# Kernel optimization log

Measured on AMD Instinct MI355X. Metric: run time of the kernel, lower is better.

The kernel has to match this reference:

```python
import jax, jax.numpy as jnp
import numpy as np

N = 50000          # nodes
E = 800000         # edges (avg degree 16)
IN, HID, OUT = 128, 32, 64
H1, H2, H3 = 4, 4, 6
NEG_SLOPE = 0.2


def setup_inputs() -> dict:
    key = jax.random.key(0)
    ks = jax.random.split(key, 18)

    def p(k, shape, fan_in):
        return (jax.random.normal(k, shape, jnp.float32) / np.sqrt(fan_in)).astype(jnp.float32)

    return {
        "x": jax.random.normal(ks[0], (N, IN), jnp.float32),
        "src": jax.random.randint(ks[1], (E,), 0, N, jnp.int32),
        "dst": jax.random.randint(ks[2], (E,), 0, N, jnp.int32),
        # layer 1: IN -> (H1, HID)
        "W1": p(ks[3], (IN, H1 * HID), IN),
        "al1": p(ks[4], (H1, HID), HID),
        "ar1": p(ks[5], (H1, HID), HID),
        "b1": jnp.zeros((H1 * HID,), jnp.float32),
        # layer 2: H1*HID -> (H2, HID), residual (identity since H1*HID == H2*HID... == in)
        "W2": p(ks[6], (H1 * HID, H2 * HID), H1 * HID),
        "al2": p(ks[7], (H2, HID), HID),
        "ar2": p(ks[8], (H2, HID), HID),
        "b2": jnp.zeros((H2 * HID,), jnp.float32),
        # layer 3: H2*HID -> (H3, OUT), residual via linear projection
        "W3": p(ks[9], (H2 * HID, H3 * OUT), H2 * HID),
        "al3": p(ks[10], (H3, OUT), OUT),
        "ar3": p(ks[11], (H3, OUT), OUT),
        "b3": jnp.zeros((H3 * OUT,), jnp.float32),
        "Wres3": p(ks[12], (H2 * HID, H3 * OUT), H2 * HID),
    }


def _gat_layer(h, W, al, ar, b, src, dst, H, D, resval=None):
    # DGL GATConv: proj, per-edge attention logits, leaky-relu, edge softmax
    # over destination neighborhoods, weighted gather-scatter aggregation.
    feat = (h @ W).reshape(N, H, D)                     # [N,H,D]
    el = jnp.sum(feat * al, axis=-1)                    # [N,H]
    er = jnp.sum(feat * ar, axis=-1)                    # [N,H]
    e = jax.nn.leaky_relu(el[src] + er[dst], NEG_SLOPE) # [E,H]
    # numerically-stable segment softmax over dst
    m = jax.ops.segment_max(e, dst, num_segments=N)     # [N,H]
    ex = jnp.exp(e - m[dst])
    s = jax.ops.segment_sum(ex, dst, num_segments=N)    # [N,H]
    a = ex / s[dst]                                     # [E,H]
    msg = feat[src] * a[..., None]                      # [E,H,D]
    rst = jax.ops.segment_sum(msg, dst, num_segments=N) # [N,H,D]
    if resval is not None:
        rst = rst + resval
    return rst + b.reshape(1, H, D)


def reference(x, src, dst, W1, al1, ar1, b1, W2, al2, ar2, b2,
              W3, al3, ar3, b3, Wres3):
    h = jax.nn.elu(_gat_layer(x, W1, al1, ar1, b1, src, dst, H1, HID))
    h = h.reshape(N, H1 * HID)
    h2 = jax.nn.elu(_gat_layer(h, W2, al2, ar2, b2, src, dst, H2, HID,
                               resval=h.reshape(N, H2, HID)))
    h2 = h2.reshape(N, H2 * HID)
    h3 = _gat_layer(h2, W3, al3, ar3, b3, src, dst, H3, OUT,
                    resval=(h2 @ Wres3).reshape(N, H3, OUT))
    return h3.mean(axis=1)                              # [N,OUT]
```

## Files before the change

kernel.cpp:

```cpp
#include <hip/hip_runtime.h>
#include <hip/hip_bf16.h>


#define NODES 50000
#define EDGES 800000
#define NEG 0.2f

typedef __attribute__((ext_vector_type(8))) short bh8;
typedef __attribute__((ext_vector_type(4))) float f4;

__device__ __forceinline__ float leaky(float e) { return e > 0.f ? e : NEG * e; }
__device__ __forceinline__ float blo(unsigned u) { return __uint_as_float(u << 16); }
__device__ __forceinline__ float bhi(unsigned u) { return __uint_as_float(u & 0xffff0000u); }
__device__ __forceinline__ unsigned f2bf(float f) {
    unsigned u = __float_as_uint(f);
    return (u + 0x7fffu + ((u >> 16) & 1u)) >> 16;
}
__device__ __forceinline__ void pk2(float a, float b, unsigned& hi, unsigned& lo) {
    unsigned ha = f2bf(a), hb = f2bf(b);
    float ra = a - __uint_as_float(ha << 16);
    float rb = b - __uint_as_float(hb << 16);
    hi = ha | (hb << 16);
    lo = f2bf(ra) | (f2bf(rb) << 16);
}

#define SW(row, bc) (((row) << 8) + ((bc) ^ (((row) & 7) << 4)))

__global__ void k_cast(const float* __restrict__ in, unsigned short* __restrict__ outb, int n4) {
    int gid = blockIdx.x * blockDim.x + threadIdx.x;
    if (gid >= n4) return;
    float4 v = *reinterpret_cast<const float4*>(in + (size_t)gid * 4);
    unsigned u0 = f2bf(v.x) | (f2bf(v.y) << 16);
    unsigned u1 = f2bf(v.z) | (f2bf(v.w) << 16);
    *reinterpret_cast<uint2*>(outb + (size_t)gid * 4) = make_uint2(u0, u1);
}

__global__ void k_prepw(const float* __restrict__ W, unsigned short* __restrict__ WT, int F) {
    int gid = blockIdx.x * blockDim.x + threadIdx.x;
    if (gid >= 128 * F) return;
    int k = gid / F, f = gid - k * F;
    WT[(size_t)f * 128 + k] = (unsigned short)f2bf(W[gid]);
}

__global__ void k_prep_bt2(const float* __restrict__ W3, const float* __restrict__ Wres3,
                           unsigned short* __restrict__ BT2) {
    int gid = blockIdx.x * blockDim.x + threadIdx.x;
    if (gid >= 64 * 896) return;
    int d = gid / 896, k = gid - d * 896;
    float v;
    if (k < 768) {
        v = W3[(size_t)(k & 127) * 384 + (k >> 7) * 64 + d];
    } else {
        int kr = k - 768;
        v = 0.f;
#pragma unroll
        for (int h = 0; h < 6; ++h) v += Wres3[(size_t)kr * 384 + h * 64 + d];
    }
    BT2[(size_t)d * 896 + k] = (unsigned short)f2bf(v);
}

__global__ void k_prep_alr3(const float* __restrict__ W3, const float* __restrict__ al3,
                            const float* __restrict__ ar3, float* __restrict__ al3c,
                            float* __restrict__ ar3c) {
    int gid = blockIdx.x * blockDim.x + threadIdx.x;
    if (gid >= 1536) return;
    int g = (gid < 768) ? gid : gid - 768;
    int h = g >> 7, k = g & 127;
    const float* a = (gid < 768) ? al3 : ar3;
    float s = 0.f;
#pragma unroll
    for (int d = 0; d < 64; ++d) s += W3[(size_t)k * 384 + h * 64 + d] * a[h * 64 + d];
    if (gid < 768) al3c[g] = s; else ar3c[g] = s;
}

__global__ void k_prep_mb(const float* __restrict__ b3, float* __restrict__ mb) {
    int d = threadIdx.x;
    if (d >= 64) return;
    float s = 0.f;
#pragma unroll
    for (int h = 0; h < 6; ++h) s += b3[h * 64 + d];
    mb[d] = s * (1.f / 6.f);
}

__global__ void k_hist2(const int* __restrict__ dst, int* __restrict__ cnt,
                        int* __restrict__ rank, int e) {
    int gid = blockIdx.x * blockDim.x + threadIdx.x;
    if (gid < e) rank[gid] = atomicAdd(&cnt[dst[gid]], 1);
}

__global__ void k_bsum(const int* __restrict__ deg, int* __restrict__ bsum, int n) {
    __shared__ int sm[256];
    int t = threadIdx.x;
    int i = blockIdx.x * 256 + t;
    sm[t] = (i < n) ? deg[i] : 0;
    __syncthreads();
#pragma unroll
    for (int off = 128; off > 0; off >>= 1) {
        if (t < off) sm[t] += sm[t + off];
        __syncthreads();
    }
    if (t == 0) bsum[blockIdx.x] = sm[0];
}

__global__ void k_bscan(const int* __restrict__ bsum, int* __restrict__ bpre, int nb) {
    __shared__ int sm[256];
    int t = threadIdx.x;
    int v = (t < nb) ? bsum[t] : 0;
    sm[t] = v;
    __syncthreads();
    for (int off = 1; off < 256; off <<= 1) {
        int u = (t >= off) ? sm[t - off] : 0;
        __syncthreads();
        sm[t] += u;
        __syncthreads();
    }
    if (t < nb) bpre[t] = sm[t] - v;
}

__global__ void k_offs(const int* __restrict__ deg, const int* __restrict__ bpre,
                       int* __restrict__ offs, int n, int e) {
    __shared__ int sm[256];
    int t = threadIdx.x;
    int i = blockIdx.x * 256 + t;
    int v = (i < n) ? deg[i] : 0;
    sm[t] = v;
    __syncthreads();
    for (int off = 1; off < 256; off <<= 1) {
        int u = (t >= off) ? sm[t - off] : 0;
        __syncthreads();
        sm[t] += u;
        __syncthreads();
    }
    if (i < n) offs[i] = bpre[blockIdx.x] + sm[t] - v;
    if (i == 0) offs[n] = e;
}

__global__ void k_fill2(const int* __restrict__ src, const int* __restrict__ dst,
                        const int* __restrict__ offs, const int* __restrict__ rank,
                        int2* __restrict__ csr2, int e) {
    int gid = blockIdx.x * blockDim.x + threadIdx.x;
    if (gid < e) {
        int d = dst[gid];
        int pos = offs[d] + rank[gid];
        csr2[pos] = make_int2(src[gid], d);
    }
}

__global__ void k_ew4(const int2* __restrict__ csr2, const float* __restrict__ el,
                      const float* __restrict__ er, unsigned short* __restrict__ aw, int e) {
    int gid = blockIdx.x * blockDim.x + threadIdx.x;
    if (gid >= e) return;
    int2 sd = csr2[gid];
    float4 l4 = *reinterpret_cast<const float4*>(el + (size_t)sd.x * 4);
    float4 r4 = *reinterpret_cast<const float4*>(er + (size_t)sd.y * 4);
    float w0 = __expf(leaky(l4.x + r4.x));
    float w1 = __expf(leaky(l4.y + r4.y));
    float w2 = __expf(leaky(l4.z + r4.z));
    float w3 = __expf(leaky(l4.w + r4.w));
    unsigned u0 = f2bf(w0) | (f2bf(w1) << 16);
    unsigned u1 = f2bf(w2) | (f2bf(w3) << 16);
    *reinterpret_cast<uint2*>(aw + (size_t)gid * 4) = make_uint2(u0, u1);
}

__global__ void k_ew6(const int2* __restrict__ csr2, const float* __restrict__ el,
                      const float* __restrict__ er, unsigned short* __restrict__ aw, int e) {
    int gid = blockIdx.x * blockDim.x + threadIdx.x;
    if (gid >= e) return;
    int2 sd = csr2[gid];
    const float2* lp = reinterpret_cast<const float2*>(el + (size_t)sd.x * 6);
    const float2* rp = reinterpret_cast<const float2*>(er + (size_t)sd.y * 6);
    float2 l0 = lp[0], l1 = lp[1], l2 = lp[2];
    float2 r0 = rp[0], r1 = rp[1], r2 = rp[2];
    unsigned w01 = f2bf(__expf(leaky(l0.x + r0.x))) | (f2bf(__expf(leaky(l0.y + r0.y))) << 16);
    unsigned w23 = f2bf(__expf(leaky(l1.x + r1.x))) | (f2bf(__expf(leaky(l1.y + r1.y))) << 16);
    unsigned w45 = f2bf(__expf(leaky(l2.x + r2.x))) | (f2bf(__expf(leaky(l2.y + r2.y))) << 16);
    unsigned char* wb = reinterpret_cast<unsigned char*>(aw) + (size_t)gid * 12;
    *reinterpret_cast<unsigned*>(wb + 0) = w01;
    *reinterpret_cast<unsigned*>(wb + 4) = w23;
    *reinterpret_cast<unsigned*>(wb + 8) = w45;
}

__global__ void k_denom4(const unsigned short* __restrict__ aw,
                         const int* __restrict__ offs, float* __restrict__ inv4, int n) {
    int gid = blockIdx.x * blockDim.x + threadIdx.x;
    if (gid >= n) return;
    int o0 = offs[gid], o1 = offs[gid + 1];
    float s0 = 0.f, s1 = 0.f, s2 = 0.f, s3 = 0.f;
    for (int p = o0; p < o1; ++p) {
        uint2 wu = *reinterpret_cast<const uint2*>(aw + (size_t)p * 4);
        s0 += blo(wu.x); s1 += bhi(wu.x);
        s2 += blo(wu.y); s3 += bhi(wu.y);
    }
    float4 r = (o1 > o0) ? make_float4(1.f / s0, 1.f / s1, 1.f / s2, 1.f / s3)
                         : make_float4(0.f, 0.f, 0.f, 0.f);
    *reinterpret_cast<float4*>(inv4 + (size_t)gid * 4) = r;
}

__global__ void k_denom6(const unsigned short* __restrict__ aw,
                         const int* __restrict__ offs, float* __restrict__ inv6, int n) {
    int gid = blockIdx.x * blockDim.x + threadIdx.x;
    if (gid >= n) return;
    int o0 = offs[gid], o1 = offs[gid + 1];
    float s[6] = {0.f, 0.f, 0.f, 0.f, 0.f, 0.f};
    const unsigned char* awb = reinterpret_cast<const unsigned char*>(aw);
    for (int p = o0; p < o1; ++p) {
        const unsigned char* wb = awb + (size_t)p * 12;
        unsigned w01 = *reinterpret_cast<const unsigned*>(wb + 0);
        unsigned w23 = *reinterpret_cast<const unsigned*>(wb + 4);
        unsigned w45 = *reinterpret_cast<const unsigned*>(wb + 8);
        s[0] += blo(w01); s[1] += bhi(w01);
        s[2] += blo(w23); s[3] += bhi(w23);
        s[4] += blo(w45); s[5] += bhi(w45);
    }
    bool has = o1 > o0;
    float* o = inv6 + (size_t)gid * 6;
#pragma unroll
    for (int h = 0; h < 6; ++h) o[h] = has ? 1.f / s[h] : 0.f;
}

__global__ __launch_bounds__(256) void k_mgemm128(const unsigned short* __restrict__ A,
                                                  const unsigned short* __restrict__ BT,
                                                  unsigned short* __restrict__ C0,
                                                  int nrows) {
    __shared__ char Alds[64 * 256];
    __shared__ char Blds[64 * 256];
    const int t  = threadIdx.x;
    const int n0 = blockIdx.x * 64;
    const int w  = t >> 6;
    const int l  = t & 63;
    const int lr = l & 15;
    const int lk = l >> 4;

    {
        int col8 = (t & 15) * 8;
        int bc   = col8 * 2;
#pragma unroll
        for (int p = 0; p < 4; ++p) {
            int row = p * 16 + (t >> 4);
            int gr  = n0 + row;
            uint4 v = make_uint4(0, 0, 0, 0);
            if (gr < nrows) v = *reinterpret_cast<const uint4*>(A + (size_t)gr * 128 + col8);
            *reinterpret_cast<uint4*>(Alds + SW(row, bc)) = v;
        }
    }

    const int rbase = (w & 1) * 32;
    const int cbase = (w >> 1) * 32;

    for (int ct = 0; ct < 2; ++ct) {
        __syncthreads();
        {
            int col8 = (t & 15) * 8;
            int bc   = col8 * 2;
#pragma unroll
            for (int p = 0; p < 4; ++p) {
                int row = p * 16 + (t >> 4);
                uint4 v = *reinterpret_cast<const uint4*>(BT + (size_t)(ct * 64 + row) * 128 + col8);
                *reinterpret_cast<uint4*>(Blds + SW(row, bc)) = v;
            }
        }
        __syncthreads();

        f4 acc00 = {0.f, 0.f, 0.f, 0.f}, acc01 = {0.f, 0.f, 0.f, 0.f};
        f4 acc10 = {0.f, 0.f, 0.f, 0.f}, acc11 = {0.f, 0.f, 0.f, 0.f};
#pragma unroll
        for (int kk = 0; kk < 4; ++kk) {
            int bck = kk * 64 + lk * 16;
            bh8 a0 = *reinterpret_cast<const bh8*>(Alds + SW(rbase + lr, bck));
            bh8 a1 = *reinterpret_cast<const bh8*>(Alds + SW(rbase + 16 + lr, bck));
            bh8 b0 = *reinterpret_cast<const bh8*>(Blds + SW(cbase + lr, bck));
            bh8 b1 = *reinterpret_cast<const bh8*>(Blds + SW(cbase + 16 + lr, bck));
            acc00 = __builtin_amdgcn_mfma_f32_16x16x32_bf16(a0, b0, acc00, 0, 0, 0);
            acc01 = __builtin_amdgcn_mfma_f32_16x16x32_bf16(a0, b1, acc01, 0, 0, 0);
            acc10 = __builtin_amdgcn_mfma_f32_16x16x32_bf16(a1, b0, acc10, 0, 0, 0);
            acc11 = __builtin_amdgcn_mfma_f32_16x16x32_bf16(a1, b1, acc11, 0, 0, 0);
        }

        const f4* accs[4] = {&acc00, &acc01, &acc10, &acc11};
#pragma unroll
        for (int m = 0; m < 2; ++m) {
#pragma unroll
            for (int j = 0; j < 4; ++j) {
                int gr = n0 + rbase + m * 16 + lk * 4 + j;
                if (gr >= nrows) continue;
#pragma unroll
                for (int n = 0; n < 2; ++n) {
                    float v = (*accs[m * 2 + n])[j];
                    C0[(size_t)gr * 128 + ct * 64 + cbase + n * 16 + lr] = (unsigned short)f2bf(v);
                }
            }
        }
    }
}

__global__ __launch_bounds__(256) void k_mtail3(const float* __restrict__ zf,
                                                const unsigned short* __restrict__ h2b,
                                                const unsigned short* __restrict__ BT2,
                                                const float* __restrict__ mb,
                                                float* __restrict__ out, int nrows) {
    __shared__ char Ahi[128 * 256];
    __shared__ char Alo[128 * 256];
    __shared__ char Blds[64 * 256];
    const int t  = threadIdx.x;
    const int n0 = blockIdx.x * 128;
    const int w  = t >> 6;
    const int l  = t & 63;
    const int lr = l & 15;
    const int lk = l >> 4;
    const int rbase = w * 32;

    f4 acc00 = {0,0,0,0}, acc01 = {0,0,0,0}, acc02 = {0,0,0,0}, acc03 = {0,0,0,0};
    f4 acc10 = {0,0,0,0}, acc11 = {0,0,0,0}, acc12 = {0,0,0,0}, acc13 = {0,0,0,0};

    for (int kt = 0; kt < 7; ++kt) {
        __syncthreads();
        {
            int col8 = (t & 15) * 8;
            int bc   = col8 * 2;
            int rr   = t >> 4;
#pragma unroll
            for (int p = 0; p < 8; ++p) {
                int row = p * 16 + rr;
                int gr  = n0 + row;
                if (kt < 6) {
                    float4 v0 = make_float4(0.f, 0.f, 0.f, 0.f);
                    float4 v1 = make_float4(0.f, 0.f, 0.f, 0.f);
                    if (gr < nrows) {
                        const float* ap = zf + (size_t)gr * 768 + kt * 128 + col8;
                        v0 = *reinterpret_cast<const float4*>(ap);
                        v1 = *reinterpret_cast<const float4*>(ap + 4);
                    }
                    unsigned h0, l0, h1, l1, h2_, l2_, h3, l3;
                    pk2(v0.x, v0.y, h0, l0);
                    pk2(v0.z, v0.w, h1, l1);
                    pk2(v1.x, v1.y, h2_, l2_);
                    pk2(v1.z, v1.w, h3, l3);
                    *reinterpret_cast<uint4*>(Ahi + SW(row, bc)) = make_uint4(h0, h1, h2_, h3);
                    *reinterpret_cast<uint4*>(Alo + SW(row, bc)) = make_uint4(l0, l1, l2_, l3);
                } else {
                    uint4 v = make_uint4(0, 0, 0, 0);
                    if (gr < nrows)
                        v = *reinterpret_cast<const uint4*>(h2b + (size_t)gr * 128 + col8);
                    *reinterpret_cast<uint4*>(Ahi + SW(row, bc)) = v;
                }
            }
#pragma unroll
            for (int p = 0; p < 4; ++p) {
                int row = p * 16 + rr;
                uint4 v = *reinterpret_cast<const uint4*>(BT2 + (size_t)row * 896 + kt * 128 + col8);
                *reinterpret_cast<uint4*>(Blds + SW(row, bc)) = v;
            }
        }
        __syncthreads();
#pragma unroll
        for (int kk = 0; kk < 4; ++kk) {
            int bck = kk * 64 + lk * 16;
            bh8 b0 = *reinterpret_cast<const bh8*>(Blds + SW(0 * 16 + lr, bck));
            bh8 b1 = *reinterpret_cast<const bh8*>(Blds + SW(1 * 16 + lr, bck));
            bh8 b2 = *reinterpret_cast<const bh8*>(Blds + SW(2 * 16 + lr, bck));
            bh8 b3 = *reinterpret_cast<const bh8*>(Blds + SW(3 * 16 + lr, bck));
            bh8 a0 = *reinterpret_cast<const bh8*>(Ahi + SW(rbase + lr, bck));
            bh8 a1 = *reinterpret_cast<const bh8*>(Ahi + SW(rbase + 16 + lr, bck));
            acc00 = __builtin_amdgcn_mfma_f32_16x16x32_bf16(a0, b0, acc00, 0, 0, 0);
            acc01 = __builtin_amdgcn_mfma_f32_16x16x32_bf16(a0, b1, acc01, 0, 0, 0);
            acc02 = __builtin_amdgcn_mfma_f32_16x16x32_bf16(a0, b2, acc02, 0, 0, 0);
            acc03 = __builtin_amdgcn_mfma_f32_16x16x32_bf16(a0, b3, acc03, 0, 0, 0);
            acc10 = __builtin_amdgcn_mfma_f32_16x16x32_bf16(a1, b0, acc10, 0, 0, 0);
            acc11 = __builtin_amdgcn_mfma_f32_16x16x32_bf16(a1, b1, acc11, 0, 0, 0);
            acc12 = __builtin_amdgcn_mfma_f32_16x16x32_bf16(a1, b2, acc12, 0, 0, 0);
            acc13 = __builtin_amdgcn_mfma_f32_16x16x32_bf16(a1, b3, acc13, 0, 0, 0);
            if (kt < 6) {
                bh8 c0 = *reinterpret_cast<const bh8*>(Alo + SW(rbase + lr, bck));
                bh8 c1 = *reinterpret_cast<const bh8*>(Alo + SW(rbase + 16 + lr, bck));
                acc00 = __builtin_amdgcn_mfma_f32_16x16x32_bf16(c0, b0, acc00, 0, 0, 0);
                acc01 = __builtin_amdgcn_mfma_f32_16x16x32_bf16(c0, b1, acc01, 0, 0, 0);
                acc02 = __builtin_amdgcn_mfma_f32_16x16x32_bf16(c0, b2, acc02, 0, 0, 0);
                acc03 = __builtin_amdgcn_mfma_f32_16x16x32_bf16(c0, b3, acc03, 0, 0, 0);
                acc10 = __builtin_amdgcn_mfma_f32_16x16x32_bf16(c1, b0, acc10, 0, 0, 0);
                acc11 = __builtin_amdgcn_mfma_f32_16x16x32_bf16(c1, b1, acc11, 0, 0, 0);
                acc12 = __builtin_amdgcn_mfma_f32_16x16x32_bf16(c1, b2, acc12, 0, 0, 0);
                acc13 = __builtin_amdgcn_mfma_f32_16x16x32_bf16(c1, b3, acc13, 0, 0, 0);
            }
        }
    }

    const f4* accs[2][4] = {{&acc00, &acc01, &acc02, &acc03},
                            {&acc10, &acc11, &acc12, &acc13}};
#pragma unroll
    for (int m = 0; m < 2; ++m) {
#pragma unroll
        for (int j = 0; j < 4; ++j) {
            int gr = n0 + rbase + m * 16 + lk * 4 + j;
            if (gr >= nrows) continue;
#pragma unroll
            for (int n = 0; n < 4; ++n) {
                int col = n * 16 + lr;
                float v = (*accs[m][n])[j];
                out[(size_t)gr * 64 + col] = v * (1.f / 6.f) + mb[col];
            }
        }
    }
}

template <int H, int D>
__global__ void k_elr_bf(const unsigned short* __restrict__ feat,
                         const float* __restrict__ al, const float* __restrict__ ar,
                         float* __restrict__ el, float* __restrict__ er, int total) {
    int gid = blockIdx.x * blockDim.x + threadIdx.x;
    if (gid >= total) return;
    int n = gid / H, h = gid - n * H;
    const uint4* f = reinterpret_cast<const uint4*>(feat + (size_t)n * (H * D) + h * D);
    const float4* a = reinterpret_cast<const float4*>(al + h * D);
    const float4* r = reinterpret_cast<const float4*>(ar + h * D);
    float sl = 0.f, sr = 0.f;
#pragma unroll
    for (int j = 0; j < D / 8; ++j) {
        uint4 v = f[j];
        float4 a0 = a[2 * j], a1 = a[2 * j + 1];
        float4 r0 = r[2 * j], r1 = r[2 * j + 1];
        float x0 = blo(v.x), x1 = bhi(v.x), x2 = blo(v.y), x3 = bhi(v.y);
        float x4 = blo(v.z), x5 = bhi(v.z), x6 = blo(v.w), x7 = bhi(v.w);
        sl += x0 * a0.x + x1 * a0.y + x2 * a0.z + x3 * a0.w +
              x4 * a1.x + x5 * a1.y + x6 * a1.z + x7 * a1.w;
        sr += x0 * r0.x + x1 * r0.y + x2 * r0.z + x3 * r0.w +
              x4 * r1.x + x5 * r1.y + x6 * r1.z + x7 * r1.w;
    }
    el[gid] = sl;
    er[gid] = sr;
}

__global__ void k_elr3(const unsigned short* __restrict__ h2b,
                       const float* __restrict__ al3c, const float* __restrict__ ar3c,
                       float* __restrict__ el, float* __restrict__ er, int total) {
    int gid = blockIdx.x * blockDim.x + threadIdx.x;
    if (gid >= total) return;
    int n = gid / 6, h = gid - n * 6;
    const uint4* f = reinterpret_cast<const uint4*>(h2b + (size_t)n * 128);
    const float4* a = reinterpret_cast<const float4*>(al3c + h * 128);
    const float4* r = reinterpret_cast<const float4*>(ar3c + h * 128);
    float sl = 0.f, sr = 0.f;
#pragma unroll
    for (int j = 0; j < 16; ++j) {
        uint4 v = f[j];
        float4 a0 = a[2 * j], a1 = a[2 * j + 1];
        float4 r0 = r[2 * j], r1 = r[2 * j + 1];
        float x0 = blo(v.x), x1 = bhi(v.x), x2 = blo(v.y), x3 = bhi(v.y);
        float x4 = blo(v.z), x5 = bhi(v.z), x6 = blo(v.w), x7 = bhi(v.w);
        sl += x0 * a0.x + x1 * a0.y + x2 * a0.z + x3 * a0.w +
              x4 * a1.x + x5 * a1.y + x6 * a1.z + x7 * a1.w;
        sr += x0 * r0.x + x1 * r0.y + x2 * r0.z + x3 * r0.w +
              x4 * r1.x + x5 * r1.y + x6 * r1.z + x7 * r1.w;
    }
    el[gid] = sl;
    er[gid] = sr;
}

template <bool HASRES, bool WRITEF32>
__global__ __launch_bounds__(256) void k_aggr128d(
    const unsigned short* __restrict__ feat, const int2* __restrict__ csr2,
    const int* __restrict__ offs, const unsigned short* __restrict__ aw,
    const float* __restrict__ inv4, const float* __restrict__ bias,
    const float* __restrict__ resf, unsigned short* __restrict__ outb,
    float* __restrict__ outf, int nnodes) {
    int node = blockIdx.x * 4 + (threadIdx.x >> 6);
    if (node >= nnodes) return;
    int l = threadIdx.x & 63;
    int half = l >> 5;
    int ll = l & 31;
    int h = ll >> 3;
    int o0 = offs[node], o1 = offs[node + 1];
    float acc0 = 0.f, acc1 = 0.f, acc2 = 0.f, acc3 = 0.f;
    int nt = (o1 - o0 + 1) >> 1;
#pragma unroll 2
    for (int t = 0; t < nt; ++t) {
        int ei = o0 + 2 * t + half;
        int pos = (ei < o1) ? ei : EDGES;
        uint2 wu = *reinterpret_cast<const uint2*>(aw + (size_t)pos * 4);
        unsigned uw = (h & 2) ? wu.y : wu.x;
        float w = (h & 1) ? bhi(uw) : blo(uw);
        int sidx = csr2[pos].x;
        uint2 u = *reinterpret_cast<const uint2*>(feat + (size_t)sidx * 128 + 4 * ll);
        acc0 = fmaf(w, blo(u.x), acc0);
        acc1 = fmaf(w, bhi(u.x), acc1);
        acc2 = fmaf(w, blo(u.y), acc2);
        acc3 = fmaf(w, bhi(u.y), acc3);
    }
    acc0 += __shfl_xor(acc0, 32);
    acc1 += __shfl_xor(acc1, 32);
    acc2 += __shfl_xor(acc2, 32);
    acc3 += __shfl_xor(acc3, 32);
    float inv = inv4[(size_t)node * 4 + h];
    int f = 4 * ll;
    float4 bi = *reinterpret_cast<const float4*>(bias + f);
    float r0 = acc0 * inv + bi.x;
    float r1 = acc1 * inv + bi.y;
    float r2 = acc2 * inv + bi.z;
    float r3 = acc3 * inv + bi.w;
    if (HASRES) {
        float4 rv = *reinterpret_cast<const float4*>(resf + (size_t)node * 128 + f);
        r0 += rv.x; r1 += rv.y; r2 += rv.z; r3 += rv.w;
    }
    r0 = (r0 > 0.f) ? r0 : (__expf(r0) - 1.f);
    r1 = (r1 > 0.f) ? r1 : (__expf(r1) - 1.f);
    r2 = (r2 > 0.f) ? r2 : (__expf(r2) - 1.f);
    r3 = (r3 > 0.f) ? r3 : (__expf(r3) - 1.f);
    if (half == 0) {
        unsigned u0 = f2bf(r0) | (f2bf(r1) << 16);
        unsigned u1 = f2bf(r2) | (f2bf(r3) << 16);
        *reinterpret_cast<uint2*>(outb + (size_t)node * 128 + f) = make_uint2(u0, u1);
        if (WRITEF32)
            *reinterpret_cast<float4*>(outf + (size_t)node * 128 + f) =
                make_float4(r0, r1, r2, r3);
    }
}

__global__ __launch_bounds__(256) void k_aggrZ3(
    const unsigned short* __restrict__ h2b, const int2* __restrict__ csr2,
    const int* __restrict__ offs, const unsigned short* __restrict__ aw6,
    const float* __restrict__ inv6, float* __restrict__ zf, int nnodes) {
    int node = blockIdx.x * 4 + (threadIdx.x >> 6);
    if (node >= nnodes) return;
    int l = threadIdx.x & 63;
    int half = l >> 5;
    int ll = l & 31;
    float acc[6][4];
#pragma unroll
    for (int h = 0; h < 6; ++h)
#pragma unroll
        for (int j = 0; j < 4; ++j) acc[h][j] = 0.f;
    int o0 = offs[node], o1 = offs[node + 1];
    int nt = (o1 - o0 + 1) >> 1;
    const unsigned char* awb = reinterpret_cast<const unsigned char*>(aw6);
#pragma unroll 2
    for (int t = 0; t < nt; ++t) {
        int ei = o0 + 2 * t + half;
        int pos = (ei < o1) ? ei : EDGES;
        const unsigned char* wb = awb + (size_t)pos * 12;
        unsigned w01 = *reinterpret_cast<const unsigned*>(wb + 0);
        unsigned w23 = *reinterpret_cast<const unsigned*>(wb + 4);
        unsigned w45 = *reinterpret_cast<const unsigned*>(wb + 8);
        float wv[6] = {blo(w01), bhi(w01), blo(w23), bhi(w23), blo(w45), bhi(w45)};
        int sidx = csr2[pos].x;
        uint2 u = *reinterpret_cast<const uint2*>(h2b + (size_t)sidx * 128 + 4 * ll);
        float f0 = blo(u.x), f1 = bhi(u.x), f2 = blo(u.y), f3 = bhi(u.y);
#pragma unroll
        for (int h = 0; h < 6; ++h) {
            acc[h][0] = fmaf(wv[h], f0, acc[h][0]);
            acc[h][1] = fmaf(wv[h], f1, acc[h][1]);
            acc[h][2] = fmaf(wv[h], f2, acc[h][2]);
            acc[h][3] = fmaf(wv[h], f3, acc[h][3]);
        }
    }
#pragma unroll
    for (int h = 0; h < 6; ++h)
#pragma unroll
        for (int j = 0; j < 4; ++j) acc[h][j] += __shfl_xor(acc[h][j], 32);
    if (half == 0) {
        float2 i01 = *reinterpret_cast<const float2*>(inv6 + (size_t)node * 6 + 0);
        float2 i23 = *reinterpret_cast<const float2*>(inv6 + (size_t)node * 6 + 2);
        float2 i45 = *reinterpret_cast<const float2*>(inv6 + (size_t)node * 6 + 4);
        float iv[6] = {i01.x, i01.y, i23.x, i23.y, i45.x, i45.y};
#pragma unroll
        for (int h = 0; h < 6; ++h) {
            *reinterpret_cast<float4*>(zf + (size_t)node * 768 + h * 128 + 4 * ll) =
                make_float4(acc[h][0] * iv[h], acc[h][1] * iv[h],
                            acc[h][2] * iv[h], acc[h][3] * iv[h]);
        }
    }
}

extern "C" void kernel_launch(void* const* d_in, const int* in_sizes, int n_in,
                              void* d_out, int out_size, void* d_ws, size_t ws_size,
                              hipStream_t stream) {
    const float* x     = (const float*)d_in[0];
    const int*   src   = (const int*)d_in[1];
    const int*   dst   = (const int*)d_in[2];
    const float* W1    = (const float*)d_in[3];
    const float* al1   = (const float*)d_in[4];
    const float* ar1   = (const float*)d_in[5];
    const float* b1    = (const float*)d_in[6];
    const float* W2    = (const float*)d_in[7];
    const float* al2   = (const float*)d_in[8];
    const float* ar2   = (const float*)d_in[9];
    const float* b2    = (const float*)d_in[10];
    const float* W3    = (const float*)d_in[11];
    const float* al3   = (const float*)d_in[12];
    const float* ar3   = (const float*)d_in[13];
    const float* b3    = (const float*)d_in[14];
    const float* Wres3 = (const float*)d_in[15];
    float* out = (float*)d_out;

    const int N = NODES, E = EDGES;
    const int NB = (N + 255) / 256;

    char*  ws = (char*)d_ws;
    size_t o  = 0;
    auto alloc = [&](size_t bytes) {
        size_t r = o;
        o += (bytes + 255) & ~(size_t)255;
        return r;
    };
    int*            offs  = (int*)(ws + alloc((size_t)(N + 1) * 4));
    int*            cnt   = (int*)(ws + alloc((size_t)N * 4));
    int2*           csr2  = (int2*)(ws + alloc((size_t)(E + 1) * 8));
    float*          el    = (float*)(ws + alloc((size_t)N * 6 * 4));
    float*          er    = (float*)(ws + alloc((size_t)N * 6 * 4));
    unsigned short* aw    = (unsigned short*)(ws + alloc((size_t)(E + 1) * 6 * 2));
    float*          inv   = (float*)(ws + alloc((size_t)N * 6 * 4));
    unsigned short* h2b   = (unsigned short*)(ws + alloc((size_t)N * 128 * 2));
    unsigned short* w1t   = (unsigned short*)(ws + alloc((size_t)128 * 128 * 2));
    unsigned short* w2t   = (unsigned short*)(ws + alloc((size_t)128 * 128 * 2));
    unsigned short* bt2   = (unsigned short*)(ws + alloc((size_t)64 * 896 * 2));
    float*          al3c  = (float*)(ws + alloc((size_t)768 * 4));
    float*          ar3c  = (float*)(ws + alloc((size_t)768 * 4));
    float*          mb    = (float*)(ws + alloc((size_t)64 * 4));
    int*            bsum  = (int*)(ws + alloc((size_t)256 * 4));
    int*            bpre  = (int*)(ws + alloc((size_t)256 * 4));
    char* U = ws + alloc((size_t)N * 768 * 4);
    unsigned short* xb    = (unsigned short*)(U);
    unsigned short* featb = (unsigned short*)(U + (size_t)N * 128 * 2);
    unsigned short* h1b   = (unsigned short*)(U + (size_t)N * 256 * 2);
    float*          h1f   = (float*)(U + (size_t)N * 384 * 2);
    int*            rank  = (int*)(U + (size_t)64 * 1024 * 1024);
    float*          zf    = (float*)(U);

    const int gE = (E + 255) / 256;
    const int g4 = (N * 4 + 255) / 256;
    const int g6 = (N * 6 + 255) / 256;
    const int gN = (N + 255) / 256;
    const int gA = (N + 3) / 4;
    const int gG = (N + 63) / 64;
    const int gT = (N + 127) / 128;

    k_cast<<<(N * 128 / 4 + 255) / 256, 256, 0, stream>>>(x, xb, N * 128 / 4);
    k_prepw<<<(128 * 128 + 255) / 256, 256, 0, stream>>>(W1, w1t, 128);
    k_prepw<<<(128 * 128 + 255) / 256, 256, 0, stream>>>(W2, w2t, 128);
    k_prep_bt2<<<(64 * 896 + 255) / 256, 256, 0, stream>>>(W3, Wres3, bt2);
    k_prep_alr3<<<6, 256, 0, stream>>>(W3, al3, ar3, al3c, ar3c);
    k_prep_mb<<<1, 64, 0, stream>>>(b3, mb);

    hipMemsetAsync(csr2 + E, 0, 8, stream);
    hipMemsetAsync((char*)aw + (size_t)E * 8, 0, 8, stream);
    hipMemsetAsync((char*)aw + (size_t)E * 12, 0, 12, stream);

    hipMemsetAsync(cnt, 0, (size_t)N * 4, stream);
    k_hist2<<<gE, 256, 0, stream>>>(dst, cnt, rank, E);
    k_bsum<<<NB, 256, 0, stream>>>(cnt, bsum, N);
    k_bscan<<<1, 256, 0, stream>>>(bsum, bpre, NB);
    k_offs<<<NB, 256, 0, stream>>>(cnt, bpre, offs, N, E);
    k_fill2<<<gE, 256, 0, stream>>>(src, dst, offs, rank, csr2, E);

    k_mgemm128<<<gG, 256, 0, stream>>>(xb, w1t, featb, N);
    k_elr_bf<4, 32><<<g4, 256, 0, stream>>>(featb, al1, ar1, el, er, N * 4);
    k_ew4<<<gE, 256, 0, stream>>>(csr2, el, er, aw, E);
    k_denom4<<<gN, 256, 0, stream>>>(aw, offs, inv, N);
    k_aggr128d<false, true><<<gA, 256, 0, stream>>>(featb, csr2, offs, aw, inv, b1,
                                                    nullptr, h1b, h1f, N);

    k_mgemm128<<<gG, 256, 0, stream>>>(h1b, w2t, featb, N);
    k_elr_bf<4, 32><<<g4, 256, 0, stream>>>(featb, al2, ar2, el, er, N * 4);
    k_ew4<<<gE, 256, 0, stream>>>(csr2, el, er, aw, E);
    k_denom4<<<gN, 256, 0, stream>>>(aw, offs, inv, N);
    k_aggr128d<true, false><<<gA, 256, 0, stream>>>(featb, csr2, offs, aw, inv, b2,
                                                    h1f, h2b, nullptr, N);

    k_elr3<<<g6, 256, 0, stream>>>(h2b, al3c, ar3c, el, er, N * 6);
    k_ew6<<<gE, 256, 0, stream>>>(csr2, el, er, aw, E);
    k_denom6<<<gN, 256, 0, stream>>>(aw, offs, inv, N);
    k_aggrZ3<<<gA, 256, 0, stream>>>(h2b, csr2, offs, aw, inv, zf, N);
    k_mtail3<<<gT, 256, 0, stream>>>(zf, h2b, bt2, mb, out, N);
}
```

Before: 389.7 us.

## Fuse layer-3 aggregation with tail GEMM via shared-memory staging

Merges the layer-3 gather aggregation kernel and the tail MFMA GEMM into a single kernel. Each 512-thread block aggregates 32 nodes into a shared-memory fp32 tile and then runs the split-bf16 GEMM straight from LDS. This drops the 768-float-per-node global round trip through zf (about 150MB written and read back). In exchange the block uses roughly 99KB of LDS, which limits occupancy during the latency-bound gather phase, and B fragments are loaded straight from global memory without reuse across blocks.

After: 446.9 us. 14.7% more time.

```diff
diff --git a/kernel.cpp b/kernel.cpp
--- a/kernel.cpp
+++ b/kernel.cpp
@@ -15,13 +15,6 @@
 __device__ __forceinline__ unsigned f2bf(float f) {
     unsigned u = __float_as_uint(f);
     return (u + 0x7fffu + ((u >> 16) & 1u)) >> 16;
-}
-__device__ __forceinline__ void pk2(float a, float b, unsigned& hi, unsigned& lo) {
-    unsigned ha = f2bf(a), hb = f2bf(b);
-    float ra = a - __uint_as_float(ha << 16);
-    float rb = b - __uint_as_float(hb << 16);
-    hi = ha | (hb << 16);
-    lo = f2bf(ra) | (f2bf(rb) << 16);
 }
 
 #define SW(row, bc) (((row) << 8) + ((bc) ^ (((row) & 7) << 4)))
@@ -288,115 +281,6 @@
                     float v = (*accs[m * 2 + n])[j];
                     C0[(size_t)gr * 128 + ct * 64 + cbase + n * 16 + lr] = (unsigned short)f2bf(v);
                 }
-            }
-        }
-    }
-}
-
-__global__ __launch_bounds__(256) void k_mtail3(const float* __restrict__ zf,
-                                                const unsigned short* __restrict__ h2b,
-                                                const unsigned short* __restrict__ BT2,
-                                                const float* __restrict__ mb,
-                                                float* __restrict__ out, int nrows) {
-    __shared__ char Ahi[128 * 256];
-    __shared__ char Alo[128 * 256];
-    __shared__ char Blds[64 * 256];
-    const int t  = threadIdx.x;
-    const int n0 = blockIdx.x * 128;
-    const int w  = t >> 6;
-    const int l  = t & 63;
-    const int lr = l & 15;
-    const int lk = l >> 4;
-    const int rbase = w * 32;
-
-    f4 acc00 = {0,0,0,0}, acc01 = {0,0,0,0}, acc02 = {0,0,0,0}, acc03 = {0,0,0,0};
-    f4 acc10 = {0,0,0,0}, acc11 = {0,0,0,0}, acc12 = {0,0,0,0}, acc13 = {0,0,0,0};
-
-    for (int kt = 0; kt < 7; ++kt) {
-        __syncthreads();
-        {
-            int col8 = (t & 15) * 8;
-            int bc   = col8 * 2;
-            int rr   = t >> 4;
-#pragma unroll
-            for (int p = 0; p < 8; ++p) {
-                int row = p * 16 + rr;
-                int gr  = n0 + row;
-                if (kt < 6) {
-                    float4 v0 = make_float4(0.f, 0.f, 0.f, 0.f);
-                    float4 v1 = make_float4(0.f, 0.f, 0.f, 0.f);
-                    if (gr < nrows) {
-                        const float* ap = zf + (size_t)gr * 768 + kt * 128 + col8;
-                        v0 = *reinterpret_cast<const float4*>(ap);
-                        v1 = *reinterpret_cast<const float4*>(ap + 4);
-                    }
-                    unsigned h0, l0, h1, l1, h2_, l2_, h3, l3;
-                    pk2(v0.x, v0.y, h0, l0);
-                    pk2(v0.z, v0.w, h1, l1);
-                    pk2(v1.x, v1.y, h2_, l2_);
-                    pk2(v1.z, v1.w, h3, l3);
-                    *reinterpret_cast<uint4*>(Ahi + SW(row, bc)) = make_uint4(h0, h1, h2_, h3);
-                    *reinterpret_cast<uint4*>(Alo + SW(row, bc)) = make_uint4(l0, l1, l2_, l3);
-                } else {
-                    uint4 v = make_uint4(0, 0, 0, 0);
-                    if (gr < nrows)
-                        v = *reinterpret_cast<const uint4*>(h2b + (size_t)gr * 128 + col8);
-                    *reinterpret_cast<uint4*>(Ahi + SW(row, bc)) = v;
-                }
-            }
-#pragma unroll
-            for (int p = 0; p < 4; ++p) {
-                int row = p * 16 + rr;
-                uint4 v = *reinterpret_cast<const uint4*>(BT2 + (size_t)row * 896 + kt * 128 + col8);
-                *reinterpret_cast<uint4*>(Blds + SW(row, bc)) = v;
-            }
-        }
-        __syncthreads();
-#pragma unroll
-        for (int kk = 0; kk < 4; ++kk) {
-            int bck = kk * 64 + lk * 16;
-            bh8 b0 = *reinterpret_cast<const bh8*>(Blds + SW(0 * 16 + lr, bck));
-            bh8 b1 = *reinterpret_cast<const bh8*>(Blds + SW(1 * 16 + lr, bck));
-            bh8 b2 = *reinterpret_cast<const bh8*>(Blds + SW(2 * 16 + lr, bck));
-            bh8 b3 = *reinterpret_cast<const bh8*>(Blds + SW(3 * 16 + lr, bck));
-            bh8 a0 = *reinterpret_cast<const bh8*>(Ahi + SW(rbase + lr, bck));
-            bh8 a1 = *reinterpret_cast<const bh8*>(Ahi + SW(rbase + 16 + lr, bck));
-            acc00 = __builtin_amdgcn_mfma_f32_16x16x32_bf16(a0, b0, acc00, 0, 0, 0);
-            acc01 = __builtin_amdgcn_mfma_f32_16x16x32_bf16(a0, b1, acc01, 0, 0, 0);
-            acc02 = __builtin_amdgcn_mfma_f32_16x16x32_bf16(a0, b2, acc02, 0, 0, 0);
-            acc03 = __builtin_amdgcn_mfma_f32_16x16x32_bf16(a0, b3, acc03, 0, 0, 0);
-            acc10 = __builtin_amdgcn_mfma_f32_16x16x32_bf16(a1, b0, acc10, 0, 0, 0);
-            acc11 = __builtin_amdgcn_mfma_f32_16x16x32_bf16(a1, b1, acc11, 0, 0, 0);
-            acc12 = __builtin_amdgcn_mfma_f32_16x16x32_bf16(a1, b2, acc12, 0, 0, 0);
-            acc13 = __builtin_amdgcn_mfma_f32_16x16x32_bf16(a1, b3, acc13, 0, 0, 0);
-            if (kt < 6) {
-                bh8 c0 = *reinterpret_cast<const bh8*>(Alo + SW(rbase + lr, bck));
-                bh8 c1 = *reinterpret_cast<const bh8*>(Alo + SW(rbase + 16 + lr, bck));
-                acc00 = __builtin_amdgcn_mfma_f32_16x16x32_bf16(c0, b0, acc00, 0, 0, 0);
-                acc01 = __builtin_amdgcn_mfma_f32_16x16x32_bf16(c0, b1, acc01, 0, 0, 0);
-                acc02 = __builtin_amdgcn_mfma_f32_16x16x32_bf16(c0, b2, acc02, 0, 0, 0);
-                acc03 = __builtin_amdgcn_mfma_f32_16x16x32_bf16(c0, b3, acc03, 0, 0, 0);
-                acc10 = __builtin_amdgcn_mfma_f32_16x16x32_bf16(c1, b0, acc10, 0, 0, 0);
-                acc11 = __builtin_amdgcn_mfma_f32_16x16x32_bf16(c1, b1, acc11, 0, 0, 0);
-                acc12 = __builtin_amdgcn_mfma_f32_16x16x32_bf16(c1, b2, acc12, 0, 0, 0);
-                acc13 = __builtin_amdgcn_mfma_f32_16x16x32_bf16(c1, b3, acc13, 0, 0, 0);
-            }
-        }
-    }
-
-    const f4* accs[2][4] = {{&acc00, &acc01, &acc02, &acc03},
-                            {&acc10, &acc11, &acc12, &acc13}};
-#pragma unroll
-    for (int m = 0; m < 2; ++m) {
-#pragma unroll
-        for (int j = 0; j < 4; ++j) {
-            int gr = n0 + rbase + m * 16 + lk * 4 + j;
-            if (gr >= nrows) continue;
-#pragma unroll
-            for (int n = 0; n < 4; ++n) {
-                int col = n * 16 + lr;
-                float v = (*accs[m][n])[j];
-                out[(size_t)gr * 64 + col] = v * (1.f / 6.f) + mb[col];
             }
         }
     }
@@ -514,58 +398,117 @@
     }
 }
 
-__global__ __launch_bounds__(256) void k_aggrZ3(
+#define ZSTRIDE 772
+__global__ __launch_bounds__(512) void k_fuse3(
     const unsigned short* __restrict__ h2b, const int2* __restrict__ csr2,
     const int* __restrict__ offs, const unsigned short* __restrict__ aw6,
-    const float* __restrict__ inv6, float* __restrict__ zf, int nnodes) {
-    int node = blockIdx.x * 4 + (threadIdx.x >> 6);
-    if (node >= nnodes) return;
-    int l = threadIdx.x & 63;
-    int half = l >> 5;
-    int ll = l & 31;
-    float acc[6][4];
-#pragma unroll
-    for (int h = 0; h < 6; ++h)
-#pragma unroll
-        for (int j = 0; j < 4; ++j) acc[h][j] = 0.f;
-    int o0 = offs[node], o1 = offs[node + 1];
-    int nt = (o1 - o0 + 1) >> 1;
+    const float* __restrict__ inv6, const unsigned short* __restrict__ BT2,
+    const float* __restrict__ mb, float* __restrict__ out, int nnodes) {
+    __shared__ float zsm[32][ZSTRIDE];
+    const int t = threadIdx.x;
+    const int w = t >> 6;
+    const int l = t & 63;
+    const int half = l >> 5;
+    const int ll = l & 31;
+    const int n0 = blockIdx.x * 32;
     const unsigned char* awb = reinterpret_cast<const unsigned char*>(aw6);
-#pragma unroll 2
-    for (int t = 0; t < nt; ++t) {
-        int ei = o0 + 2 * t + half;
-        int pos = (ei < o1) ? ei : EDGES;
-        const unsigned char* wb = awb + (size_t)pos * 12;
-        unsigned w01 = *reinterpret_cast<const unsigned*>(wb + 0);
-        unsigned w23 = *reinterpret_cast<const unsigned*>(wb + 4);
-        unsigned w45 = *reinterpret_cast<const unsigned*>(wb + 8);
-        float wv[6] = {blo(w01), bhi(w01), blo(w23), bhi(w23), blo(w45), bhi(w45)};
-        int sidx = csr2[pos].x;
-        uint2 u = *reinterpret_cast<const uint2*>(h2b + (size_t)sidx * 128 + 4 * ll);
-        float f0 = blo(u.x), f1 = bhi(u.x), f2 = blo(u.y), f3 = bhi(u.y);
-#pragma unroll
-        for (int h = 0; h < 6; ++h) {
-            acc[h][0] = fmaf(wv[h], f0, acc[h][0]);
-            acc[h][1] = fmaf(wv[h], f1, acc[h][1]);
-            acc[h][2] = fmaf(wv[h], f2, acc[h][2]);
-            acc[h][3] = fmaf(wv[h], f3, acc[h][3]);
-        }
-    }
-#pragma unroll
-    for (int h = 0; h < 6; ++h)
-#pragma unroll
-        for (int j = 0; j < 4; ++j) acc[h][j] += __shfl_xor(acc[h][j], 32);
-    if (half == 0) {
-        float2 i01 = *reinterpret_cast<const float2*>(inv6 + (size_t)node * 6 + 0);
-        float2 i23 = *reinterpret_cast<const float2*>(inv6 + (size_t)node * 6 + 2);
-        float2 i45 = *reinterpret_cast<const float2*>(inv6 + (size_t)node * 6 + 4);
-        float iv[6] = {i01.x, i01.y, i23.x, i23.y, i45.x, i45.y};
-#pragma unroll
-        for (int h = 0; h < 6; ++h) {
-            *reinterpret_cast<float4*>(zf + (size_t)node * 768 + h * 128 + 4 * ll) =
-                make_float4(acc[h][0] * iv[h], acc[h][1] * iv[h],
-                            acc[h][2] * iv[h], acc[h][3] * iv[h]);
-        }
+
+    for (int i = 0; i < 4; ++i) {
+        int ln = w * 4 + i;
+        int node = n0 + ln;
+        if (node >= nnodes) break;
+        float acc[6][4];
+#pragma unroll
+        for (int h = 0; h < 6; ++h)
+#pragma unroll
+            for (int j = 0; j < 4; ++j) acc[h][j] = 0.f;
+        int o0 = offs[node], o1 = offs[node + 1];
+        int nt = (o1 - o0 + 1) >> 1;
+#pragma unroll 4
+        for (int e = 0; e < nt; ++e) {
+            int ei = o0 + 2 * e + half;
+            int pos = (ei < o1) ? ei : EDGES;
+            const unsigned char* wb = awb + (size_t)pos * 12;
+            unsigned w01 = *reinterpret_cast<const unsigned*>(wb + 0);
+            unsigned w23 = *reinterpret_cast<const unsigned*>(wb + 4);
+            unsigned w45 = *reinterpret_cast<const unsigned*>(wb + 8);
+            float wv[6] = {blo(w01), bhi(w01), blo(w23), bhi(w23), blo(w45), bhi(w45)};
+            int sidx = csr2[pos].x;
+            uint2 u = *reinterpret_cast<const uint2*>(h2b + (size_t)sidx * 128 + 4 * ll);
+            float f0 = blo(u.x), f1 = bhi(u.x), f2 = blo(u.y), f3 = bhi(u.y);
+#pragma unroll
+            for (int h = 0; h < 6; ++h) {
+                acc[h][0] = fmaf(wv[h], f0, acc[h][0]);
+                acc[h][1] = fmaf(wv[h], f1, acc[h][1]);
+                acc[h][2] = fmaf(wv[h], f2, acc[h][2]);
+                acc[h][3] = fmaf(wv[h], f3, acc[h][3]);
+            }
+        }
+#pragma unroll
+        for (int h = 0; h < 6; ++h)
+#pragma unroll
+            for (int j = 0; j < 4; ++j) acc[h][j] += __shfl_xor(acc[h][j], 32);
+        if (half == 0) {
+            float2 i01 = *reinterpret_cast<const float2*>(inv6 + (size_t)node * 6 + 0);
+            float2 i23 = *reinterpret_cast<const float2*>(inv6 + (size_t)node * 6 + 2);
+            float2 i45 = *reinterpret_cast<const float2*>(inv6 + (size_t)node * 6 + 4);
+            float iv[6] = {i01.x, i01.y, i23.x, i23.y, i45.x, i45.y};
+#pragma unroll
+            for (int h = 0; h < 6; ++h) {
+                *reinterpret_cast<float4*>(&zsm[ln][h * 128 + 4 * ll]) =
+                    make_float4(acc[h][0] * iv[h], acc[h][1] * iv[h],
+                                acc[h][2] * iv[h], acc[h][3] * iv[h]);
+            }
+        }
+    }
+    __syncthreads();
+
+    const int lr = l & 15;
+    const int lk = l >> 4;
+    const int rowfrag = (w & 1) * 16;
+    const int colfrag = (w >> 1) * 16;
+    const int colrow = colfrag + lr;
+    f4 acc = {0.f, 0.f, 0.f, 0.f};
+
+    for (int kt = 0; kt < 6; ++kt) {
+#pragma unroll
+        for (int kk = 0; kk < 4; ++kk) {
+            int koff = kt * 128 + kk * 32 + lk * 8;
+            bh8 b = *reinterpret_cast<const bh8*>(BT2 + (size_t)colrow * 896 + koff);
+            const float* zp = &zsm[rowfrag + lr][koff];
+            bh8 ahi, alo;
+#pragma unroll
+            for (int j = 0; j < 8; ++j) {
+                float zv = zp[j];
+                unsigned hb = f2bf(zv);
+                float rem = zv - __uint_as_float(hb << 16);
+                ahi[j] = (short)hb;
+                alo[j] = (short)f2bf(rem);
+            }
+            acc = __builtin_amdgcn_mfma_f32_16x16x32_bf16(ahi, b, acc, 0, 0, 0);
+            acc = __builtin_amdgcn_mfma_f32_16x16x32_bf16(alo, b, acc, 0, 0, 0);
+        }
+    }
+    {
+        int gr = n0 + rowfrag + lr;
+        bool valid = gr < nnodes;
+#pragma unroll
+        for (int kk = 0; kk < 4; ++kk) {
+            int koff = 768 + kk * 32 + lk * 8;
+            bh8 b = *reinterpret_cast<const bh8*>(BT2 + (size_t)colrow * 896 + koff);
+            bh8 a = {0, 0, 0, 0, 0, 0, 0, 0};
+            if (valid)
+                a = *reinterpret_cast<const bh8*>(h2b + (size_t)gr * 128 + kk * 32 + lk * 8);
+            acc = __builtin_amdgcn_mfma_f32_16x16x32_bf16(a, b, acc, 0, 0, 0);
+        }
+    }
+
+    float mbv = mb[colfrag + lr];
+#pragma unroll
+    for (int j = 0; j < 4; ++j) {
+        int gr = n0 + rowfrag + lk * 4 + j;
+        if (gr < nnodes)
+            out[(size_t)gr * 64 + colfrag + lr] = acc[j] * (1.f / 6.f) + mbv;
     }
 }
 
@@ -616,13 +559,12 @@
     float*          mb    = (float*)(ws + alloc((size_t)64 * 4));
     int*            bsum  = (int*)(ws + alloc((size_t)256 * 4));
     int*            bpre  = (int*)(ws + alloc((size_t)256 * 4));
-    char* U = ws + alloc((size_t)N * 768 * 4);
+    char* U = ws + alloc((size_t)70 * 1024 * 1024);
     unsigned short* xb    = (unsigned short*)(U);
     unsigned short* featb = (unsigned short*)(U + (size_t)N * 128 * 2);
     unsigned short* h1b   = (unsigned short*)(U + (size_t)N * 256 * 2);
     float*          h1f   = (float*)(U + (size_t)N * 384 * 2);
     int*            rank  = (int*)(U + (size_t)64 * 1024 * 1024);
-    float*          zf    = (float*)(U);
 
     const int gE = (E + 255) / 256;
     const int g4 = (N * 4 + 255) / 256;
@@ -630,7 +572,7 @@
     const int gN = (N + 255) / 256;
     const int gA = (N + 3) / 4;
     const int gG = (N + 63) / 64;
-    const int gT = (N + 127) / 128;
+    const int gF = (N + 31) / 32;
 
     k_cast<<<(N * 128 / 4 + 255) / 256, 256, 0, stream>>>(x, xb, N * 128 / 4);
     k_prepw<<<(128 * 128 + 255) / 256, 256, 0, stream>>>(W1, w1t, 128);
@@ -667,6 +609,5 @@
     k_elr3<<<g6, 256, 0, stream>>>(h2b, al3c, ar3c, el, er, N * 6);
     k_ew6<<<gE, 256, 0, stream>>>(csr2, el, er, aw, E);
     k_denom6<<<gN, 256, 0, stream>>>(aw, offs, inv, N);
-    k_aggrZ3<<<gA, 256, 0, stream>>>(h2b, csr2, offs, aw, inv, zf, N);
-    k_mtail3<<<gT, 256, 0, stream>>>(zf, h2b, bt2, mb, out, N);
-}
+    k_fuse3<<<gF, 512, 0, stream>>>(h2b, csr2, offs, aw, inv, bt2, mb, out, N);
+}
```
